# Kernel optimization log

Measured on AMD Instinct MI355X. Metric: run time of the kernel, lower is better.

Reference implementation:

```python
import jax, jax.numpy as jnp
import numpy as np

H, P, T = 256, 16, 4      # hidden_size, maxout_pool_size, max_dec_steps
B, M = 32, 600            # batch, document length

def _lstm_cell(x, h, c, W_ih, W_hh, b_ih, b_hh):
    g = x @ W_ih.T + b_ih + h @ W_hh.T + b_hh
    i, f, gg, o = jnp.split(g, 4, axis=1)  # torch gate order i,f,g,o
    c = jax.nn.sigmoid(f) * c + jax.nn.sigmoid(i) * jnp.tanh(gg)
    h = jax.nn.sigmoid(o) * jnp.tanh(c)
    return h, c

def _maxout(h, U, u_cat, mask_mult, W_lin, W1, b1, W2, b2, W12, b12):
    b, m, _ = U.shape
    r = jnp.tanh(jnp.concatenate([h, u_cat], axis=1) @ W_lin.T)                  # [b,H]
    m1_in = jnp.concatenate([U, jnp.broadcast_to(r[:, None, :], (b, m, H))], 2)  # [b,m,3H]
    m1 = (m1_in @ W1.T + b1).reshape(b, m, H, P).max(-1)                         # [b,m,H]
    m2 = (m1 @ W2.T + b2).reshape(b, m, H, P).max(-1)                            # [b,m,H]
    alpha = (jnp.concatenate([m1, m2], axis=2) @ W12.T + b12).max(-1)            # [b,m]
    return jax.nn.log_softmax(alpha + mask_mult, axis=1)

def _forward(U, d_mask, span, W_ih, W_hh, b_ih, b_hh,
             Ws_lin, Ws_m1, bs_m1, Ws_m2, bs_m2, Ws_m12, bs_m12,
             We_lin, We_m1, be_m1, We_m2, be_m2, We_m12, be_m12):
    b, m, _ = U.shape
    idxb = jnp.arange(b)
    mask_mult = (1.0 - d_mask.astype(U.dtype)) * -1e30
    s_i = jnp.zeros(b, jnp.int32)
    e_i = (jnp.sum(d_mask, 1) - 1).astype(jnp.int32)
    s_tgt, e_tgt = span[:, 0], span[:, 1]
    h = jnp.zeros((b, H), U.dtype)
    c = jnp.zeros((b, H), U.dtype)
    mask_s = mask_e = None
    res_s, res_e, res_ms, res_me, losses = [], [], [], [], []
    u_s = U[idxb, s_i]
    for t in range(T):
        u_e = U[idxb, e_i]
        u_cat = jnp.concatenate([u_s, u_e], axis=1)
        h, c = _lstm_cell(u_cat, h, c, W_ih, W_hh, b_ih, b_hh)
        # start pointer
        lsm = _maxout(h, U, u_cat, mask_mult, Ws_lin, Ws_m1, bs_m1, Ws_m2, bs_m2, Ws_m12, bs_m12)
        idx = jnp.argmax(lsm, axis=1).astype(jnp.int32)
        if t == 0:
            mask_s = jnp.ones(b, bool)
        else:
            idx = idx * mask_s.astype(jnp.int32)
            prev = s_i * mask_s.astype(jnp.int32)
            mask_s = idx != prev
        loss_s = jnp.mean(-jnp.take_along_axis(lsm, s_tgt[:, None], 1)[:, 0]) * mask_s.astype(U.dtype)
        s_i = idx
        u_s = U[idxb, s_i]
        # end pointer
        u_cat2 = jnp.concatenate([u_s, u_e], axis=1)
        lsm_e = _maxout(h, U, u_cat2, mask_mult, We_lin, We_m1, be_m1, We_m2, be_m2, We_m12, be_m12)
        idx_e = jnp.argmax(lsm_e, axis=1).astype(jnp.int32)
        if t == 0:
            mask_e = jnp.ones(b, bool)
        else:
            idx_e = idx_e * mask_e.astype(jnp.int32)
            prev_e = e_i * mask_e.astype(jnp.int32)
            mask_e = idx_e != prev_e
        loss_e = jnp.mean(-jnp.take_along_axis(lsm_e, e_tgt[:, None], 1)[:, 0]) * mask_e.astype(U.dtype)
        e_i = idx_e
        losses.append(loss_s + loss_e)
        res_s.append(s_i); res_ms.append(mask_s)
        res_e.append(e_i); res_me.append(mask_e)
    pos_s = jnp.sum(jnp.stack(res_ms, 1).astype(jnp.int32), 1) - 1
    p1 = jnp.take_along_axis(jnp.stack(res_s, 1), pos_s[:, None], 1)[:, 0]
    pos_e = jnp.sum(jnp.stack(res_me, 1).astype(jnp.int32), 1) - 1
    p2 = jnp.take_along_axis(jnp.stack(res_e, 1), pos_e[:, None], 1)[:, 0]
    loss = jnp.mean(jnp.sum(jnp.stack(losses, 1), 1) / T)
    return loss, p1, p2

def setup_inputs():
    key = jax.random.key(0)
    ks = jax.random.split(key, 16)
    U = jax.random.normal(ks[0], (B, M, 2 * H), jnp.float32)
    lengths = jax.random.randint(ks[1], (B,), M // 2, M + 1)
    d_mask = (jnp.arange(M)[None, :] < lengths[:, None]).astype(jnp.int32)
    span = jax.random.randint(ks[2], (B, 2), 0, M // 2).astype(jnp.int32)
    def w(k, shape, fan_in):
        return (jax.random.normal(k, shape, jnp.float32) / np.float32(np.sqrt(fan_in)))
    b_ih = jnp.zeros(4 * H, jnp.float32).at[H:2 * H].set(1.0)  # forget-gate bias init
    params = {
        'W_ih': w(ks[3], (4 * H, 4 * H), 4 * H), 'W_hh': w(ks[4], (4 * H, H), H),
        'b_ih': b_ih, 'b_hh': jnp.zeros(4 * H, jnp.float32),
        'Ws_lin': w(ks[5], (H, 5 * H), 5 * H),
        'Ws_m1': w(ks[6], (H * P, 3 * H), 3 * H), 'bs_m1': jnp.zeros(H * P, jnp.float32),
        'Ws_m2': w(ks[7], (H * P, H), H), 'bs_m2': jnp.zeros(H * P, jnp.float32),
        'Ws_m12': w(ks[8], (P, 2 * H), 2 * H), 'bs_m12': jnp.zeros(P, jnp.float32),
        'We_lin': w(ks[9], (H, 5 * H), 5 * H),
        'We_m1': w(ks[10], (H * P, 3 * H), 3 * H), 'be_m1': jnp.zeros(H * P, jnp.float32),
        'We_m2': w(ks[11], (H * P, H), H), 'be_m2': jnp.zeros(H * P, jnp.float32),
        'We_m12': w(ks[12], (P, 2 * H), 2 * H), 'be_m12': jnp.zeros(P, jnp.float32),
    }
    return {'U': U, 'd_mask': d_mask, 'span': span, **params}

def reference(U, d_mask, span, W_ih, W_hh, b_ih, b_hh,
              Ws_lin, Ws_m1, bs_m1, Ws_m2, bs_m2, Ws_m12, bs_m12,
              We_lin, We_m1, be_m1, We_m2, be_m2, We_m12, be_m12):
    return _forward(U, d_mask, span, W_ih, W_hh, b_ih, b_hh,
                    Ws_lin, Ws_m1, bs_m1, Ws_m2, bs_m2, Ws_m12, bs_m12,
                    We_lin, We_m1, be_m1, We_m2, be_m2, We_m12, be_m12)
```

## Files before the change

kernel.cpp:

```cpp
#include <hip/hip_runtime.h>
#include <math.h>

namespace {

typedef unsigned short u16;
typedef __attribute__((ext_vector_type(4))) float f32x4;
typedef __attribute__((ext_vector_type(8))) _Float16 f16x8;
typedef __attribute__((ext_vector_type(4))) _Float16 f16x4;

constexpr int B = 32;
constexpr int M = 600;
constexpr int H = 256;
constexpr int TSTEPS = 4;
constexpr int HP = 4096;
constexpr int BM = B * M;
constexpr int TWOH = 512;
constexpr int THREEH = 768;
constexpr int FOURH = 1024;
constexpr int FIVEH = 1280;
constexpr int NTILES = BM / 128;

__device__ __forceinline__ float sigf(float x) { return 1.0f / (1.0f + expf(-x)); }

__device__ __forceinline__ void gload16(const u16* g, u16* l) {
    __builtin_amdgcn_global_load_lds(
        (const __attribute__((address_space(1))) void*)g,
        (__attribute__((address_space(3))) void*)l, 16, 0, 0);
}

__global__ void k_init(const int* __restrict__ d_mask,
                       float* __restrict__ h, float* __restrict__ c,
                       float* __restrict__ loss_vec,
                       int* __restrict__ s_i, int* __restrict__ e_i,
                       int* __restrict__ p1r, int* __restrict__ p2r)
{
    int tid = threadIdx.x;
    for (int i = tid; i < B * H; i += 256) { h[i] = 0.f; c[i] = 0.f; }
    if (tid < B) {
        loss_vec[tid] = 0.f;
        s_i[tid] = 0;
        int s = 0;
        const int* row = d_mask + tid * M;
        for (int m = 0; m < M; ++m) s += row[m];
        e_i[tid] = s - 1;
        p1r[tid] = 0; p2r[tid] = 0;
    }
}

__global__ __launch_bounds__(128) void k_flags(const int* __restrict__ d_mask,
                                               int* __restrict__ flags)
{
    int bm = blockIdx.x * 128 + threadIdx.x;
    int cnt = __syncthreads_count(d_mask[bm]);
    if (threadIdx.x == 0) flags[blockIdx.x] = (cnt == 0) ? 1 : 0;
}

__global__ __launch_bounds__(256) void k_gather(
    const float* __restrict__ U, const int* __restrict__ s_i,
    const int* __restrict__ e_i, float* __restrict__ u_cat)
{
    int idx = blockIdx.x * 256 + threadIdx.x;
    int b = idx >> 9, k = idx & 511;
    u_cat[b * FOURH + k]       = U[((size_t)b * M + s_i[b]) * TWOH + k];
    u_cat[b * FOURH + 512 + k] = U[((size_t)b * M + e_i[b]) * TWOH + k];
}

__global__ __launch_bounds__(256) void k_lstm_gemm2(
    const float* __restrict__ U, const int* __restrict__ s_i,
    const int* __restrict__ e_i, const float* __restrict__ h,
    const float* __restrict__ W_ih, const float* __restrict__ W_hh,
    const float* __restrict__ b_ih, const float* __restrict__ b_hh,
    float* __restrict__ g)
{
    int idx = blockIdx.x * 256 + threadIdx.x;
    int b = idx >> 10, j = idx & 1023;
    const float* us = U + ((size_t)b * M + s_i[b]) * TWOH;
    const float* ue = U + ((size_t)b * M + e_i[b]) * TWOH;
    float acc = 0.f;
    const float4* x4 = (const float4*)us;
    const float4* wi4 = (const float4*)(W_ih + (size_t)j * FOURH);
    #pragma unroll 4
    for (int k = 0; k < TWOH / 4; ++k) {
        float4 a = x4[k], w = wi4[k];
        acc += a.x * w.x + a.y * w.y + a.z * w.z + a.w * w.w;
    }
    const float4* y4 = (const float4*)ue;
    const float4* wi4b = wi4 + TWOH / 4;
    #pragma unroll 4
    for (int k = 0; k < TWOH / 4; ++k) {
        float4 a = y4[k], w = wi4b[k];
        acc += a.x * w.x + a.y * w.y + a.z * w.z + a.w * w.w;
    }
    const float4* h4 = (const float4*)(h + b * H);
    const float4* wh4 = (const float4*)(W_hh + (size_t)j * H);
    #pragma unroll 4
    for (int k = 0; k < H / 4; ++k) {
        float4 a = h4[k], w = wh4[k];
        acc += a.x * w.x + a.y * w.y + a.z * w.z + a.w * w.w;
    }
    g[idx] = acc + b_ih[j] + b_hh[j];
}

__global__ __launch_bounds__(256) void k_lstm_gemm(
    const float* __restrict__ u_cat, const float* __restrict__ h,
    const float* __restrict__ W_ih, const float* __restrict__ W_hh,
    const float* __restrict__ b_ih, const float* __restrict__ b_hh,
    float* __restrict__ g)
{
    int idx = blockIdx.x * 256 + threadIdx.x;
    int b = idx >> 10, j = idx & 1023;
    float acc = 0.f;
    const float4* x4 = (const float4*)(u_cat + b * FOURH);
    const float4* wi4 = (const float4*)(W_ih + (size_t)j * FOURH);
    #pragma unroll 4
    for (int k = 0; k < FOURH / 4; ++k) {
        float4 a = x4[k], w = wi4[k];
        acc += a.x * w.x + a.y * w.y + a.z * w.z + a.w * w.w;
    }
    const float4* h4 = (const float4*)(h + b * H);
    const float4* wh4 = (const float4*)(W_hh + (size_t)j * H);
    #pragma unroll 4
    for (int k = 0; k < H / 4; ++k) {
        float4 a = h4[k], w = wh4[k];
        acc += a.x * w.x + a.y * w.y + a.z * w.z + a.w * w.w;
    }
    g[idx] = acc + b_ih[j] + b_hh[j];
}

__global__ __launch_bounds__(256) void k_lstm_gates(
    const float* __restrict__ g, float* __restrict__ h, float* __restrict__ c)
{
    int idx = blockIdx.x * 256 + threadIdx.x;
    int b = idx >> 8, i = idx & (H - 1);
    const float* gr = g + b * FOURH;
    float gi = gr[i], gf = gr[H + i], gg = gr[2 * H + i], go = gr[3 * H + i];
    float cn = sigf(gf) * c[idx] + sigf(gi) * tanhf(gg);
    c[idx] = cn;
    h[idx] = sigf(go) * tanhf(cn);
}

__global__ __launch_bounds__(256) void k_r2(
    const float* __restrict__ h, const float* __restrict__ U,
    const int* __restrict__ s_i, const int* __restrict__ e_i,
    const float* __restrict__ W_lin, float* __restrict__ r)
{
    int idx = blockIdx.x * 256 + threadIdx.x;
    int b = idx >> 8, i = idx & (H - 1);
    const float* w = W_lin + (size_t)i * FIVEH;
    float acc = 0.f;
    const float4* h4 = (const float4*)(h + b * H);
    const float4* w4 = (const float4*)w;
    #pragma unroll 4
    for (int k = 0; k < H / 4; ++k) {
        float4 a = h4[k], ww = w4[k];
        acc += a.x * ww.x + a.y * ww.y + a.z * ww.z + a.w * ww.w;
    }
    const float4* x4 = (const float4*)(U + ((size_t)b * M + s_i[b]) * TWOH);
    const float4* w4b = (const float4*)(w + H);
    #pragma unroll 4
    for (int k = 0; k < TWOH / 4; ++k) {
        float4 a = x4[k], ww = w4b[k];
        acc += a.x * ww.x + a.y * ww.y + a.z * ww.z + a.w * ww.w;
    }
    const float4* y4 = (const float4*)(U + ((size_t)b * M + e_i[b]) * TWOH);
    const float4* w4c = (const float4*)(w + H + TWOH);
    #pragma unroll 4
    for (int k = 0; k < TWOH / 4; ++k) {
        float4 a = y4[k], ww = w4c[k];
        acc += a.x * ww.x + a.y * ww.y + a.z * ww.z + a.w * ww.w;
    }
    r[idx] = tanhf(acc);
}

__global__ __launch_bounds__(256) void k_r(
    const float* __restrict__ h, const float* __restrict__ u_cat,
    const float* __restrict__ W_lin, float* __restrict__ r)
{
    int idx = blockIdx.x * 256 + threadIdx.x;
    int b = idx >> 8, i = idx & (H - 1);
    const float* w = W_lin + (size_t)i * FIVEH;
    float acc = 0.f;
    const float4* h4 = (const float4*)(h + b * H);
    const float4* w4 = (const float4*)w;
    #pragma unroll 4
    for (int k = 0; k < H / 4; ++k) {
        float4 a = h4[k], ww = w4[k];
        acc += a.x * ww.x + a.y * ww.y + a.z * ww.z + a.w * ww.w;
    }
    const float4* x4 = (const float4*)(u_cat + b * FOURH);
    const float4* w4b = (const float4*)(w + H);
    #pragma unroll 4
    for (int k = 0; k < FOURH / 4; ++k) {
        float4 a = x4[k], ww = w4b[k];
        acc += a.x * ww.x + a.y * ww.y + a.z * ww.z + a.w * ww.w;
    }
    r[idx] = tanhf(acc);
}

__global__ __launch_bounds__(256) void k_rW(
    const float* __restrict__ r, const float* __restrict__ W1,
    const float* __restrict__ b1, float* __restrict__ rW)
{
    int idx = blockIdx.x * 256 + threadIdx.x;
    int b = idx >> 12, j = idx & (HP - 1);
    const float4* r4 = (const float4*)(r + b * H);
    const float4* w4 = (const float4*)(W1 + (size_t)j * THREEH + TWOH);
    float acc = 0.f;
    #pragma unroll 4
    for (int k = 0; k < H / 4; ++k) {
        float4 a = r4[k], w = w4[k];
        acc += a.x * w.x + a.y * w.y + a.z * w.z + a.w * w.w;
    }
    rW[idx] = acc + b1[j];
}

__global__ __launch_bounds__(256) void k_rW2(
    const float* __restrict__ r, const float* __restrict__ Wt,
    const float* __restrict__ b1, float* __restrict__ rW)
{
    const int b = blockIdx.y;
    const int j = blockIdx.x * 256 + threadIdx.x;
    __shared__ float sr[256];
    sr[threadIdx.x] = r[b * H + threadIdx.x];
    __syncthreads();
    float acc = b1[j];
    #pragma unroll 4
    for (int k = 0; k < H; ++k) acc += sr[k] * Wt[(size_t)k * HP + j];
    rW[(size_t)b * HP + j] = acc;
}

__global__ __launch_bounds__(256) void k_transp(
    const float* __restrict__ W, float* __restrict__ Wt)
{
    int idx = blockIdx.x * 256 + threadIdx.x;
    int k = idx >> 12, j = idx & (HP - 1);
    Wt[idx] = W[(size_t)j * THREEH + TWOH + k];
}

__global__ __launch_bounds__(256) void k_cvtH(
    const float* __restrict__ src, int ld, int Kc, _Float16* __restrict__ dst)
{
    int i4 = blockIdx.x * 256 + threadIdx.x;
    int perrow = Kc >> 2;
    int row = i4 / perrow;
    int kc = (i4 - row * perrow) << 2;
    float4 v = *(const float4*)(src + (size_t)row * ld + kc);
    f16x4 o;
    o[0] = (_Float16)v.x; o[1] = (_Float16)v.y; o[2] = (_Float16)v.z; o[3] = (_Float16)v.w;
    *(f16x4*)(dst + (size_t)row * Kc + kc) = o;
}

template <int EPI>
__global__ __launch_bounds__(256, 4) void gemmJ(
    const _Float16* __restrict__ A, const _Float16* __restrict__ Bw,
    int K, const float* __restrict__ extra, const int* __restrict__ skip,
    float* __restrict__ Cf, _Float16* __restrict__ Ch)
{
    if (skip[blockIdx.y]) return;
    __shared__ __align__(16) u16 sA[2][128 * 32];
    __shared__ __align__(16) u16 sB[2][128 * 32];
    const int tid = threadIdx.x;
    const int w = tid >> 6, lane = tid & 63;
    const int row0 = blockIdx.y * 128, col0 = blockIdx.x * 128;
    const int wm = w & 1, wn = w >> 1;

    const int r1g = tid >> 2,        k1 = (tid & 3) ^ ((r1g >> 1) & 3);
    const int r2g = (tid + 256) >> 2, k2 = ((tid + 256) & 3) ^ ((r2g >> 1) & 3);
    const size_t gA1 = (size_t)(row0 + r1g) * K + k1 * 8;
    const size_t gA2 = (size_t)(row0 + r2g) * K + k2 * 8;
    const size_t gB1 = (size_t)(col0 + r1g) * K + k1 * 8;
    const size_t gB2 = (size_t)(col0 + r2g) * K + k2 * 8;

    f32x4 acc[4][4] = {};

    gload16((const u16*)(A  + gA1), &sA[0][tid * 8]);
    gload16((const u16*)(A  + gA2), &sA[0][(tid + 256) * 8]);
    gload16((const u16*)(Bw + gB1), &sB[0][tid * 8]);
    gload16((const u16*)(Bw + gB2), &sB[0][(tid + 256) * 8]);

    const int iters = K >> 5;
    const int mrow = lane & 15;
    const int kg = lane >> 4;
    const int slot = kg ^ ((mrow >> 1) & 3);
    const int eoff = slot << 3;

    for (int it = 0; it < iters; ++it) {
        const int cur = it & 1;
        __syncthreads();
        if (it + 1 < iters) {
            const int k0n = (it + 1) << 5;
            gload16((const u16*)(A  + gA1 + k0n), &sA[1 - cur][tid * 8]);
            gload16((const u16*)(A  + gA2 + k0n), &sA[1 - cur][(tid + 256) * 8]);
            gload16((const u16*)(Bw + gB1 + k0n), &sB[1 - cur][tid * 8]);
            gload16((const u16*)(Bw + gB2 + k0n), &sB[1 - cur][(tid + 256) * 8]);
        }
        const u16* pa = &sA[cur][(wm * 64 + mrow) * 32 + eoff];
        const u16* pb = &sB[cur][(wn * 64 + mrow) * 32 + eoff];
        f16x8 fa[4], fb[4];
        #pragma unroll
        for (int f = 0; f < 4; ++f) {
            fa[f] = *(const f16x8*)(pa + f * 16 * 32);
            fb[f] = *(const f16x8*)(pb + f * 16 * 32);
        }
        #pragma unroll
        for (int i = 0; i < 4; ++i) {
            #pragma unroll
            for (int j = 0; j < 4; ++j) {
                acc[i][j] = __builtin_amdgcn_mfma_f32_16x16x32_f16(fa[i], fb[j], acc[i][j], 0, 0, 0);
            }
        }
    }

    const int cq = lane & 15, rq = lane >> 4;
    if (EPI == 4) {
        #pragma unroll
        for (int i = 0; i < 4; ++i) {
            #pragma unroll
            for (int j = 0; j < 4; ++j) {
                int col = col0 + wn * 64 + j * 16 + cq;
                #pragma unroll
                for (int rr = 0; rr < 4; ++rr) {
                    int row = row0 + wm * 64 + i * 16 + rq * 4 + rr;
                    Ch[(size_t)row * HP + col] = (_Float16)acc[i][j][rr];
                }
            }
        }
    } else if (EPI == 1) {
        #pragma unroll
        for (int j = 0; j < 4; ++j) {
            int col = col0 + wn * 64 + j * 16 + cq;
            int gcol = (col0 >> 4) + wn * 4 + j;
            float bv = extra[col];
            #pragma unroll
            for (int i = 0; i < 4; ++i) {
                #pragma unroll
                for (int rr = 0; rr < 4; ++rr) {
                    float v = acc[i][j][rr] + bv;
                    v = fmaxf(v, __shfl_xor(v, 1));
                    v = fmaxf(v, __shfl_xor(v, 2));
                    v = fmaxf(v, __shfl_xor(v, 4));
                    v = fmaxf(v, __shfl_xor(v, 8));
                    if (cq == 0) {
                        int row = row0 + wm * 64 + i * 16 + rq * 4 + rr;
                        Cf[(size_t)row * H + gcol] = v;
                    }
                }
            }
        }
    } else {
        #pragma unroll
        for (int j = 0; j < 4; ++j) {
            int col = col0 + wn * 64 + j * 16 + cq;
            int gcol = (col0 >> 4) + wn * 4 + j;
            #pragma unroll
            for (int i = 0; i < 4; ++i) {
                #pragma unroll
                for (int rr = 0; rr < 4; ++rr) {
                    int row = row0 + wm * 64 + i * 16 + rq * 4 + rr;
                    int b = row / M;
                    float v = acc[i][j][rr] + extra[(size_t)b * HP + col];
                    v = fmaxf(v, __shfl_xor(v, 1));
                    v = fmaxf(v, __shfl_xor(v, 2));
                    v = fmaxf(v, __shfl_xor(v, 4));
                    v = fmaxf(v, __shfl_xor(v, 8));
                    if (cq == 0)
                        Ch[(size_t)row * H + gcol] = (_Float16)v;
                }
            }
        }
    }
}

__global__ __launch_bounds__(256) void k_m1A16(
    const _Float16* __restrict__ A, const float* __restrict__ rW,
    _Float16* __restrict__ m1)
{
    int idx = blockIdx.x * 256 + threadIdx.x;
    int bm = idx >> 8;
    int h = idx & (H - 1);
    int b = bm / M;
    const f16x8* a8 = (const f16x8*)(A + (size_t)bm * HP + (h << 4));
    const float4* r4 = (const float4*)(rW + (size_t)b * HP + (h << 4));
    f16x8 a0 = a8[0], a1 = a8[1];
    float4 ra = r4[0], rb = r4[1], rc = r4[2], rd = r4[3];
    float mx;
    mx = fmaxf(fmaxf(fmaxf((float)a0[0] + ra.x, (float)a0[1] + ra.y),
                     fmaxf((float)a0[2] + ra.z, (float)a0[3] + ra.w)),
         fmaxf(fmaxf((float)a0[4] + rb.x, (float)a0[5] + rb.y),
               fmaxf((float)a0[6] + rb.z, (float)a0[7] + rb.w)));
    mx = fmaxf(mx,
         fmaxf(fmaxf(fmaxf((float)a1[0] + rc.x, (float)a1[1] + rc.y),
                     fmaxf((float)a1[2] + rc.z, (float)a1[3] + rc.w)),
               fmaxf(fmaxf((float)a1[4] + rd.x, (float)a1[5] + rd.y),
                     fmaxf((float)a1[6] + rd.z, (float)a1[7] + rd.w))));
    m1[idx] = (_Float16)mx;
}

template <int EPI>
__global__ __launch_bounds__(256) void gemm64(
    const float* __restrict__ Ag, int lda,
    const float* __restrict__ Bg, int ldb,
    const float* __restrict__ extra,
    float* __restrict__ C, int K, int ldc)
{
    __shared__ float As[16][68];
    __shared__ float Bs[16][68];
    const int tid = threadIdx.x;
    const int tx = tid & 15;
    const int ty = tid >> 4;
    const int row0 = blockIdx.y * 64;
    const int col0 = blockIdx.x * 64;
    const int lr = tid >> 2;
    const int lk = (tid & 3) << 2;
    const float* Aload = Ag + (size_t)(row0 + lr) * lda + lk;
    const float* Bload = Bg + (size_t)(col0 + lr) * ldb + lk;
    float acc[4][4] = {};
    for (int k0 = 0; k0 < K; k0 += 16) {
        float4 av = *(const float4*)(Aload + k0);
        float4 bv = *(const float4*)(Bload + k0);
        __syncthreads();
        As[lk + 0][lr] = av.x; As[lk + 1][lr] = av.y; As[lk + 2][lr] = av.z; As[lk + 3][lr] = av.w;
        Bs[lk + 0][lr] = bv.x; Bs[lk + 1][lr] = bv.y; Bs[lk + 2][lr] = bv.z; Bs[lk + 3][lr] = bv.w;
        __syncthreads();
        #pragma unroll
        for (int k = 0; k < 16; ++k) {
            float4 a4 = *(const float4*)(&As[k][ty << 2]);
            float4 b4 = *(const float4*)(&Bs[k][tx << 2]);
            acc[0][0] += a4.x * b4.x; acc[0][1] += a4.x * b4.y; acc[0][2] += a4.x * b4.z; acc[0][3] += a4.x * b4.w;
            acc[1][0] += a4.y * b4.x; acc[1][1] += a4.y * b4.y; acc[1][2] += a4.y * b4.z; acc[1][3] += a4.y * b4.w;
            acc[2][0] += a4.z * b4.x; acc[2][1] += a4.z * b4.y; acc[2][2] += a4.z * b4.z; acc[2][3] += a4.z * b4.w;
            acc[3][0] += a4.w * b4.x; acc[3][1] += a4.w * b4.y; acc[3][2] += a4.w * b4.z; acc[3][3] += a4.w * b4.w;
        }
    }
    if (EPI == 1) {
        const int cb = col0 + (tx << 2);
        float b0 = extra[cb], b1v = extra[cb + 1], b2v = extra[cb + 2], b3v = extra[cb + 3];
        #pragma unroll
        for (int i = 0; i < 4; ++i) {
            float mth = fmaxf(fmaxf(acc[i][0] + b0, acc[i][1] + b1v),
                              fmaxf(acc[i][2] + b2v, acc[i][3] + b3v));
            float r1 = fmaxf(mth, __shfl_xor(mth, 1));
            float r2 = fmaxf(r1, __shfl_xor(r1, 2));
            if ((tx & 3) == 0)
                C[(size_t)(row0 + (ty << 2) + i) * ldc + (col0 >> 4) + (tx >> 2)] = r2;
        }
    } else if (EPI == 2) {
        const int cb = col0 + (tx << 2);
        #pragma unroll
        for (int i = 0; i < 4; ++i) {
            int row = row0 + (ty << 2) + i;
            int b = row / M;
            const float* rw = extra + (size_t)b * HP + cb;
            float mth = fmaxf(fmaxf(acc[i][0] + rw[0], acc[i][1] + rw[1]),
                              fmaxf(acc[i][2] + rw[2], acc[i][3] + rw[3]));
            float r1 = fmaxf(mth, __shfl_xor(mth, 1));
            float r2 = fmaxf(r1, __shfl_xor(r1, 2));
            if ((tx & 3) == 0)
                C[(size_t)row * ldc + (col0 >> 4) + (tx >> 2)] = r2;
        }
    }
}

__global__ __launch_bounds__(256) void k_alpha(
    const float* __restrict__ m1, const float* __restrict__ m2,
    const float* __restrict__ W12, const float* __restrict__ b12,
    const int* __restrict__ d_mask, float* __restrict__ alpha)
{
    __shared__ float Ws[16 * 512];
    const int tid = threadIdx.x;
    for (int i = tid; i < 16 * 512; i += 256) Ws[i] = W12[i];
    __syncthreads();
    const int wave = tid >> 6, lane = tid & 63;
    const int bm = blockIdx.x * 4 + wave;
    const float* r1 = m1 + (size_t)bm * H;
    const float* r2 = m2 + (size_t)bm * H;
    float acc[16] = {};
    #pragma unroll
    for (int q = 0; q < 4; ++q) {
        int k = lane + (q << 6);
        float x = r1[k];
        #pragma unroll
        for (int p = 0; p < 16; ++p) acc[p] += x * Ws[p * 512 + k];
    }
    #pragma unroll
    for (int q = 0; q < 4; ++q) {
        int k = lane + (q << 6);
        float x = r2[k];
        #pragma unroll
        for (int p = 0; p < 16; ++p) acc[p] += x * Ws[p * 512 + 256 + k];
    }
    #pragma unroll
    for (int p = 0; p < 16; ++p) {
        float v = acc[p];
        v += __shfl_xor(v, 1);  v += __shfl_xor(v, 2);  v += __shfl_xor(v, 4);
        v += __shfl_xor(v, 8);  v += __shfl_xor(v, 16); v += __shfl_xor(v, 32);
        acc[p] = v;
    }
    if (lane == 0) {
        float mx = -INFINITY;
        #pragma unroll
        for (int p = 0; p < 16; ++p) mx = fmaxf(mx, acc[p] + b12[p]);
        alpha[bm] = d_mask[bm] ? mx : -1e30f;
    }
}

__global__ __launch_bounds__(256) void k_alpha2(
    const _Float16* __restrict__ m1, const float* __restrict__ m2,
    const float* __restrict__ W12, const float* __restrict__ b12,
    const int* __restrict__ d_mask, float* __restrict__ alpha)
{
    __shared__ float Ws[16 * 512];
    const int tid = threadIdx.x;
    for (int i = tid; i < 16 * 512; i += 256) Ws[i] = W12[i];
    __syncthreads();
    const int wave = tid >> 6, lane = tid & 63;
    const int bm0 = blockIdx.x * 16 + wave * 4;
    for (int rr = 0; rr < 4; ++rr) {
        const int bm = bm0 + rr;
        if (!d_mask[bm]) {
            if (lane == 0) alpha[bm] = -1e30f;
            continue;
        }
        const _Float16* r1 = m1 + (size_t)bm * H;
        const float* r2 = m2 + (size_t)bm * H;
        float acc[16] = {};
        #pragma unroll
        for (int q = 0; q < 4; ++q) {
            int k = lane + (q << 6);
            float x = (float)r1[k];
            #pragma unroll
            for (int p = 0; p < 16; ++p) acc[p] += x * Ws[p * 512 + k];
        }
        #pragma unroll
        for (int q = 0; q < 4; ++q) {
            int k = lane + (q << 6);
            float x = r2[k];
            #pragma unroll
            for (int p = 0; p < 16; ++p) acc[p] += x * Ws[p * 512 + 256 + k];
        }
        #pragma unroll
        for (int p = 0; p < 16; ++p) {
            float v = acc[p];
            v += __shfl_xor(v, 1);  v += __shfl_xor(v, 2);  v += __shfl_xor(v, 4);
            v += __shfl_xor(v, 8);  v += __shfl_xor(v, 16); v += __shfl_xor(v, 32);
            acc[p] = v;
        }
        if (lane == 0) {
            float mx = -INFINITY;
            #pragma unroll
            for (int p = 0; p < 16; ++p) mx = fmaxf(mx, acc[p] + b12[p]);
            alpha[bm] = mx;
        }
    }
}

__global__ __launch_bounds__(1024) void k_smu(
    const float* __restrict__ alpha, const int* __restrict__ span, int phase,
    int* __restrict__ pos, int* __restrict__ mask,
    int* __restrict__ prun, float* __restrict__ loss_vec, int t)
{
    __shared__ float s_loss[B];
    __shared__ int s_idx[B];
    const int wave = threadIdx.x >> 6, lane = threadIdx.x & 63;
    for (int b = wave; b < B; b += 16) {
        const float* row = alpha + b * M;
        float best = -INFINITY; int bidx = 0;
        for (int m = lane; m < M; m += 64) {
            float v = row[m];
            if (v > best) { best = v; bidx = m; }
        }
        #pragma unroll
        for (int off = 1; off < 64; off <<= 1) {
            float v2 = __shfl_xor(best, off);
            int i2 = __shfl_xor(bidx, off);
            if (v2 > best || (v2 == best && i2 < bidx)) { best = v2; bidx = i2; }
        }
        float ps = 0.f;
        for (int m = lane; m < M; m += 64) ps += expf(row[m] - best);
        #pragma unroll
        for (int off = 32; off > 0; off >>= 1) ps += __shfl_xor(ps, off);
        if (lane == 0) {
            float lse = best + logf(ps);
            int tgt = span[b * 2 + phase];
            s_loss[b] = -(row[tgt] - lse);
            s_idx[b] = bidx;
        }
    }
    __syncthreads();
    if (wave == 0) {
        int b = lane;
        int active = (b < B) ? 1 : 0;
        int ni = 0, nm = 0;
        if (active) {
            int id = s_idx[b];
            if (t == 0) { nm = 1; ni = id; }
            else {
                int om = mask[b];
                ni = id * om;
                int prev = pos[b] * om;
                nm = (ni != prev) ? 1 : 0;
            }
        }
        float v = active ? s_loss[b] : 0.f;
        #pragma unroll
        for (int off = 32; off > 0; off >>= 1) v += __shfl_xor(v, off);
        float S = v * (1.0f / (float)B);
        if (active) {
            pos[b] = ni;
            mask[b] = nm;
            if (nm) { prun[b] = ni; loss_vec[b] += S; }
        }
    }
}

__global__ __launch_bounds__(256) void k_softmax(
    const float* __restrict__ alpha, const int* __restrict__ span, int phase,
    float* __restrict__ loss_term, int* __restrict__ idx_out)
{
    __shared__ float sv[256];
    __shared__ int si[256];
    const int b = blockIdx.x, tid = threadIdx.x;
    const float* row = alpha + b * M;
    float best = -INFINITY; int bidx = 0;
    for (int m = tid; m < M; m += 256) {
        float v = row[m];
        if (v > best) { best = v; bidx = m; }
    }
    sv[tid] = best; si[tid] = bidx;
    __syncthreads();
    for (int s = 128; s > 0; s >>= 1) {
        if (tid < s) {
            float v2 = sv[tid + s]; int i2 = si[tid + s];
            if (v2 > sv[tid] || (v2 == sv[tid] && i2 < si[tid])) { sv[tid] = v2; si[tid] = i2; }
        }
        __syncthreads();
    }
    float bmax = sv[0]; int amax = si[0];
    __syncthreads();
    float ps = 0.f;
    for (int m = tid; m < M; m += 256) ps += expf(row[m] - bmax);
    sv[tid] = ps;
    __syncthreads();
    for (int s = 128; s > 0; s >>= 1) {
        if (tid < s) sv[tid] += sv[tid + s];
        __syncthreads();
    }
    if (tid == 0) {
        float lse = bmax + logf(sv[0]);
        int tgt = span[b * 2 + phase];
        loss_term[b] = -(row[tgt] - lse);
        idx_out[b] = amax;
    }
}

__global__ void k_update(const int* __restrict__ idx_in, const float* __restrict__ loss_term,
                         int* __restrict__ pos, int* __restrict__ mask,
                         int* __restrict__ prun, float* __restrict__ loss_vec, int t)
{
    int b = threadIdx.x;
    int active = (b < B) ? 1 : 0;
    int ni = 0, nm = 0;
    if (active) {
        int id = idx_in[b];
        if (t == 0) { nm = 1; ni = id; }
        else {
            int om = mask[b];
            ni = id * om;
            int prev = pos[b] * om;
            nm = (ni != prev) ? 1 : 0;
        }
    }
    float v = active ? loss_term[b] : 0.f;
    #pragma unroll
    for (int off = 32; off > 0; off >>= 1) v += __shfl_xor(v, off);
    float S = v * (1.0f / (float)B);
    if (active) {
        pos[b] = ni;
        mask[b] = nm;
        if (nm) { prun[b] = ni; loss_vec[b] += S; }
    }
}

__global__ void k_finalize(const float* __restrict__ loss_vec, const int* __restrict__ p1r,
                           const int* __restrict__ p2r, float* __restrict__ out)
{
    int b = threadIdx.x;
    float v = (b < B) ? loss_vec[b] : 0.f;
    #pragma unroll
    for (int off = 32; off > 0; off >>= 1) v += __shfl_xor(v, off);
    if (b == 0) out[0] = v / (float)(B * TSTEPS);
    if (b < B) {
        out[1 + b] = (float)p1r[b];
        out[1 + B + b] = (float)p2r[b];
    }
}

}

extern "C" void kernel_launch(void* const* d_in, const int* in_sizes, int n_in,
                              void* d_out, int out_size, void* d_ws, size_t ws_size,
                              hipStream_t stream)
{
    const float* U      = (const float*)d_in[0];
    const int*   d_mask = (const int*)d_in[1];
    const int*   span   = (const int*)d_in[2];
    const float* W_ih   = (const float*)d_in[3];
    const float* W_hh   = (const float*)d_in[4];
    const float* b_ih   = (const float*)d_in[5];
    const float* b_hh   = (const float*)d_in[6];
    const float* Ws_lin = (const float*)d_in[7];
    const float* Ws_m1  = (const float*)d_in[8];
    const float* bs_m1  = (const float*)d_in[9];
    const float* Ws_m2  = (const float*)d_in[10];
    const float* bs_m2  = (const float*)d_in[11];
    const float* Ws_m12 = (const float*)d_in[12];
    const float* bs_m12 = (const float*)d_in[13];
    const float* We_lin = (const float*)d_in[14];
    const float* We_m1  = (const float*)d_in[15];
    const float* be_m1  = (const float*)d_in[16];
    const float* We_m2  = (const float*)d_in[17];
    const float* be_m2  = (const float*)d_in[18];
    const float* We_m12 = (const float*)d_in[19];
    const float* be_m12 = (const float*)d_in[20];

    float* ws = (float*)d_ws;
    size_t o = 0;
    float* m2b   = ws + o; o += (size_t)BM * H;
    float* alphab= ws + o; o += BM;
    float* u_cat = ws + o; o += B * FOURH;
    float* gbuf  = ws + o; o += B * FOURH;
    float* hbuf  = ws + o; o += B * H;
    float* cbuf  = ws + o; o += B * H;
    float* rbuf  = ws + o; o += B * H;
    float* rWb   = ws + o; o += B * HP;
    float* loss_term = ws + o; o += B;
    float* loss_vec  = ws + o; o += B;
    int* ib = (int*)(ws + o); o += 8 * B + 160;
    int* idxb   = ib + 0 * B;
    int* s_i    = ib + 1 * B;
    int* e_i    = ib + 2 * B;
    int* mask_s = ib + 3 * B;
    int* mask_e = ib + 4 * B;
    int* p1r    = ib + 5 * B;
    int* p2r    = ib + 6 * B;
    int* flags  = ib + 8 * B;
    size_t o_common = (o + 3) & ~(size_t)3;

    float* m1b = ws + o_common;

    size_t p = o_common;
    float* Wt_s = ws + p; p += (size_t)H * HP;
    float* Wt_e = ws + p; p += (size_t)H * HP;
    _Float16* hs = (_Float16*)(ws + p);
    size_t q = 0;
    _Float16* Uh  = hs + q; q += (size_t)BM * TWOH;
    _Float16* W1s = hs + q; q += (size_t)HP * TWOH;
    _Float16* W1e = hs + q; q += (size_t)HP * TWOH;
    _Float16* W2s = hs + q; q += (size_t)HP * H;
    _Float16* W2e = hs + q; q += (size_t)HP * H;
    _Float16* m1b16 = hs + q; q += (size_t)BM * H;
    q = (q + 7) & ~(size_t)7;
    const size_t need2 = p * sizeof(float) + q * sizeof(_Float16);
    _Float16* A_s16 = hs + q;
    _Float16* A_e16 = A_s16 + (size_t)BM * HP;
    const size_t need15s = need2 + (size_t)BM * HP * sizeof(_Float16);
    const size_t need16  = need15s + (size_t)BM * HP * sizeof(_Float16);

    const int tier = (ws_size >= need16) ? 16
                   : (ws_size >= need15s) ? 15
                   : (ws_size >= need2) ? 2 : 3;

    k_init<<<1, 256, 0, stream>>>(d_mask, hbuf, cbuf, loss_vec, s_i, e_i, p1r, p2r);

    if (tier != 3) {
        k_flags<<<NTILES, 128, 0, stream>>>(d_mask, flags);
        k_cvtH<<<BM * TWOH / 4 / 256, 256, 0, stream>>>(U, TWOH, TWOH, Uh);
        k_cvtH<<<HP * TWOH / 4 / 256, 256, 0, stream>>>(Ws_m1, THREEH, TWOH, W1s);
        k_cvtH<<<HP * TWOH / 4 / 256, 256, 0, stream>>>(We_m1, THREEH, TWOH, W1e);
        k_cvtH<<<HP * H / 4 / 256, 256, 0, stream>>>(Ws_m2, H, H, W2s);
        k_cvtH<<<HP * H / 4 / 256, 256, 0, stream>>>(We_m2, H, H, W2e);
        k_transp<<<HP * H / 256, 256, 0, stream>>>(Ws_m1, Wt_s);
        k_transp<<<HP * H / 256, 256, 0, stream>>>(We_m1, Wt_e);

        dim3 gJ(HP / 128, NTILES);
        if (tier >= 15) {
            gemmJ<4><<<gJ, 256, 0, stream>>>(Uh, W1s, TWOH, nullptr, flags, nullptr, A_s16);
        }
        if (tier == 16) {
            gemmJ<4><<<gJ, 256, 0, stream>>>(Uh, W1e, TWOH, nullptr, flags, nullptr, A_e16);
        }

        for (int t = 0; t < TSTEPS; ++t) {
            k_lstm_gemm2<<<128, 256, 0, stream>>>(U, s_i, e_i, hbuf, W_ih, W_hh, b_ih, b_hh, gbuf);
            k_lstm_gates<<<32, 256, 0, stream>>>(gbuf, hbuf, cbuf);

            k_r2<<<32, 256, 0, stream>>>(hbuf, U, s_i, e_i, Ws_lin, rbuf);
            k_rW2<<<dim3(HP / 256, B), 256, 0, stream>>>(rbuf, Wt_s, bs_m1, rWb);
            if (tier >= 15)
                k_m1A16<<<BM * H / 256, 256, 0, stream>>>(A_s16, rWb, m1b16);
            else
                gemmJ<3><<<gJ, 256, 0, stream>>>(Uh, W1s, TWOH, rWb, flags, nullptr, m1b16);
            gemmJ<1><<<gJ, 256, 0, stream>>>(m1b16, W2s, H, bs_m2, flags, m2b, nullptr);
            k_alpha2<<<BM / 16, 256, 0, stream>>>(m1b16, m2b, Ws_m12, bs_m12, d_mask, alphab);
            k_smu<<<1, 1024, 0, stream>>>(alphab, span, 0, s_i, mask_s, p1r, loss_vec, t);

            k_r2<<<32, 256, 0, stream>>>(hbuf, U, s_i, e_i, We_lin, rbuf);
            k_rW2<<<dim3(HP / 256, B), 256, 0, stream>>>(rbuf, Wt_e, be_m1, rWb);
            if (tier == 16)
                k_m1A16<<<BM * H / 256, 256, 0, stream>>>(A_e16, rWb, m1b16);
            else
                gemmJ<3><<<gJ, 256, 0, stream>>>(Uh, W1e, TWOH, rWb, flags, nullptr, m1b16);
            gemmJ<1><<<gJ, 256, 0, stream>>>(m1b16, W2e, H, be_m2, flags, m2b, nullptr);
            k_alpha2<<<BM / 16, 256, 0, stream>>>(m1b16, m2b, We_m12, be_m12, d_mask, alphab);
            k_smu<<<1, 1024, 0, stream>>>(alphab, span, 1, e_i, mask_e, p2r, loss_vec, t);
        }
    } else {
        dim3 gemm_grid(HP / 64, BM / 64);
        for (int t = 0; t < TSTEPS; ++t) {
            k_gather<<<64, 256, 0, stream>>>(U, s_i, e_i, u_cat);
            k_lstm_gemm<<<128, 256, 0, stream>>>(u_cat, hbuf, W_ih, W_hh, b_ih, b_hh, gbuf);
            k_lstm_gates<<<32, 256, 0, stream>>>(gbuf, hbuf, cbuf);

            k_r<<<32, 256, 0, stream>>>(hbuf, u_cat, Ws_lin, rbuf);
            k_rW<<<512, 256, 0, stream>>>(rbuf, Ws_m1, bs_m1, rWb);
            gemm64<2><<<gemm_grid, 256, 0, stream>>>(U, TWOH, Ws_m1, THREEH, rWb, m1b, TWOH, H);
            gemm64<1><<<gemm_grid, 256, 0, stream>>>(m1b, H, Ws_m2, H, bs_m2, m2b, H, H);
            k_alpha<<<BM / 4, 256, 0, stream>>>(m1b, m2b, Ws_m12, bs_m12, d_mask, alphab);
            k_softmax<<<B, 256, 0, stream>>>(alphab, span, 0, loss_term, idxb);
            k_update<<<1, 64, 0, stream>>>(idxb, loss_term, s_i, mask_s, p1r, loss_vec, t);

            k_gather<<<64, 256, 0, stream>>>(U, s_i, e_i, u_cat);

            k_r<<<32, 256, 0, stream>>>(hbuf, u_cat, We_lin, rbuf);
            k_rW<<<512, 256, 0, stream>>>(rbuf, We_m1, be_m1, rWb);
            gemm64<2><<<gemm_grid, 256, 0, stream>>>(U, TWOH, We_m1, THREEH, rWb, m1b, TWOH, H);
            gemm64<1><<<gemm_grid, 256, 0, stream>>>(m1b, H, We_m2, H, be_m2, m2b, H, H);
            k_alpha<<<BM / 4, 256, 0, stream>>>(m1b, m2b, We_m12, be_m12, d_mask, alphab);
            k_softmax<<<B, 256, 0, stream>>>(alphab, span, 1, loss_term, idxb);
            k_update<<<1, 64, 0, stream>>>(idxb, loss_term, e_i, mask_e, p2r, loss_vec, t);
        }
    }

    k_finalize<<<1, 64, 0, stream>>>(loss_vec, p1r, p2r, (float*)d_out);
}
```

Baseline: 2.878 ms.

## Split r projection across lanes, tile weight transpose, store m2 as fp16

Splits the r-projection dot product four ways per output with shuffle reduction and launches four times more blocks, so the small kernel gets more parallelism. Replaces the strided weight transpose with a shared-memory tiled transpose for coalesced reads and writes. Stores the m2 maxout result as fp16 instead of fp32, which halves its write and read traffic in the alpha kernel at some cost in precision. Also hoists the per-row batch bias lookup in the gemm epilogue into two preloaded values selected by a row boundary.

Result: faster. 2.511 ms (-12.8%).

```diff
diff --git a/kernel.cpp b/kernel.cpp
--- a/kernel.cpp
+++ b/kernel.cpp
@@ -144,6 +144,34 @@
     const int* __restrict__ s_i, const int* __restrict__ e_i,
     const float* __restrict__ W_lin, float* __restrict__ r)
 {
+    int gid = blockIdx.x * 256 + threadIdx.x;
+    int out = gid >> 2;
+    int part = gid & 3;
+    int b = out >> 8, i = out & (H - 1);
+    const float4* w4 = (const float4*)(W_lin + (size_t)i * FIVEH);
+    const float4* h4 = (const float4*)(h + b * H);
+    const float4* us4 = (const float4*)(U + ((size_t)b * M + s_i[b]) * TWOH);
+    const float4* ue4 = (const float4*)(U + ((size_t)b * M + e_i[b]) * TWOH);
+    float acc = 0.f;
+    int k0 = part * 80;
+    #pragma unroll 4
+    for (int kk = k0; kk < k0 + 80; ++kk) {
+        float4 a;
+        if (kk < 64) a = h4[kk];
+        else if (kk < 192) a = us4[kk - 64];
+        else a = ue4[kk - 192];
+        float4 ww = w4[kk];
+        acc += a.x * ww.x + a.y * ww.y + a.z * ww.z + a.w * ww.w;
+    }
+    acc += __shfl_xor(acc, 1);
+    acc += __shfl_xor(acc, 2);
+    if (part == 0) r[out] = tanhf(acc);
+}
+
+__global__ __launch_bounds__(256) void k_r(
+    const float* __restrict__ h, const float* __restrict__ u_cat,
+    const float* __restrict__ W_lin, float* __restrict__ r)
+{
     int idx = blockIdx.x * 256 + threadIdx.x;
     int b = idx >> 8, i = idx & (H - 1);
     const float* w = W_lin + (size_t)i * FIVEH;
@@ -155,38 +183,6 @@
         float4 a = h4[k], ww = w4[k];
         acc += a.x * ww.x + a.y * ww.y + a.z * ww.z + a.w * ww.w;
     }
-    const float4* x4 = (const float4*)(U + ((size_t)b * M + s_i[b]) * TWOH);
-    const float4* w4b = (const float4*)(w + H);
-    #pragma unroll 4
-    for (int k = 0; k < TWOH / 4; ++k) {
-        float4 a = x4[k], ww = w4b[k];
-        acc += a.x * ww.x + a.y * ww.y + a.z * ww.z + a.w * ww.w;
-    }
-    const float4* y4 = (const float4*)(U + ((size_t)b * M + e_i[b]) * TWOH);
-    const float4* w4c = (const float4*)(w + H + TWOH);
-    #pragma unroll 4
-    for (int k = 0; k < TWOH / 4; ++k) {
-        float4 a = y4[k], ww = w4c[k];
-        acc += a.x * ww.x + a.y * ww.y + a.z * ww.z + a.w * ww.w;
-    }
-    r[idx] = tanhf(acc);
-}
-
-__global__ __launch_bounds__(256) void k_r(
-    const float* __restrict__ h, const float* __restrict__ u_cat,
-    const float* __restrict__ W_lin, float* __restrict__ r)
-{
-    int idx = blockIdx.x * 256 + threadIdx.x;
-    int b = idx >> 8, i = idx & (H - 1);
-    const float* w = W_lin + (size_t)i * FIVEH;
-    float acc = 0.f;
-    const float4* h4 = (const float4*)(h + b * H);
-    const float4* w4 = (const float4*)w;
-    #pragma unroll 4
-    for (int k = 0; k < H / 4; ++k) {
-        float4 a = h4[k], ww = w4[k];
-        acc += a.x * ww.x + a.y * ww.y + a.z * ww.z + a.w * ww.w;
-    }
     const float4* x4 = (const float4*)(u_cat + b * FOURH);
     const float4* w4b = (const float4*)(w + H);
     #pragma unroll 4
@@ -229,12 +225,24 @@
     rW[(size_t)b * HP + j] = acc;
 }
 
-__global__ __launch_bounds__(256) void k_transp(
+__global__ __launch_bounds__(256) void k_transp2(
     const float* __restrict__ W, float* __restrict__ Wt)
 {
-    int idx = blockIdx.x * 256 + threadIdx.x;
-    int k = idx >> 12, j = idx & (HP - 1);
-    Wt[idx] = W[(size_t)j * THREEH + TWOH + k];
+    __shared__ float s[32][33];
+    int j0 = (blockIdx.x & 127) << 5;
+    int k0 = (blockIdx.x >> 7) << 5;
+    int tx = threadIdx.x & 31, ty = threadIdx.x >> 5;
+    #pragma unroll
+    for (int kk = 0; kk < 4; ++kk) {
+        int jl = ty + kk * 8;
+        s[jl][tx] = W[(size_t)(j0 + jl) * THREEH + TWOH + k0 + tx];
+    }
+    __syncthreads();
+    #pragma unroll
+    for (int kk = 0; kk < 4; ++kk) {
+        int kl = ty + kk * 8;
+        Wt[(size_t)(k0 + kl) * HP + j0 + tx] = s[tx][kl];
+    }
 }
 
 __global__ __launch_bounds__(256) void k_cvtH(
@@ -342,23 +350,27 @@
                     v = fmaxf(v, __shfl_xor(v, 8));
                     if (cq == 0) {
                         int row = row0 + wm * 64 + i * 16 + rq * 4 + rr;
-                        Cf[(size_t)row * H + gcol] = v;
+                        Ch[(size_t)row * H + gcol] = (_Float16)v;
                     }
                 }
             }
         }
     } else {
+        const int rbase = row0 + wm * 64;
+        const int b0 = rbase / M;
+        const int bnd = (b0 + 1) * M;
         #pragma unroll
         for (int j = 0; j < 4; ++j) {
             int col = col0 + wn * 64 + j * 16 + cq;
             int gcol = (col0 >> 4) + wn * 4 + j;
+            float e0 = extra[(size_t)b0 * HP + col];
+            float e1 = extra[(size_t)(b0 + 1) * HP + col];
             #pragma unroll
             for (int i = 0; i < 4; ++i) {
                 #pragma unroll
                 for (int rr = 0; rr < 4; ++rr) {
-                    int row = row0 + wm * 64 + i * 16 + rq * 4 + rr;
-                    int b = row / M;
-                    float v = acc[i][j][rr] + extra[(size_t)b * HP + col];
+                    int row = rbase + i * 16 + rq * 4 + rr;
+                    float v = acc[i][j][rr] + ((row >= bnd) ? e1 : e0);
                     v = fmaxf(v, __shfl_xor(v, 1));
                     v = fmaxf(v, __shfl_xor(v, 2));
                     v = fmaxf(v, __shfl_xor(v, 4));
@@ -505,7 +517,7 @@
 }
 
 __global__ __launch_bounds__(256) void k_alpha2(
-    const _Float16* __restrict__ m1, const float* __restrict__ m2,
+    const _Float16* __restrict__ m1, const _Float16* __restrict__ m2,
     const float* __restrict__ W12, const float* __restrict__ b12,
     const int* __restrict__ d_mask, float* __restrict__ alpha)
 {
@@ -522,7 +534,7 @@
             continue;
         }
         const _Float16* r1 = m1 + (size_t)bm * H;
-        const float* r2 = m2 + (size_t)bm * H;
+        const _Float16* r2 = m2 + (size_t)bm * H;
         float acc[16] = {};
         #pragma unroll
         for (int q = 0; q < 4; ++q) {
@@ -534,7 +546,7 @@
         #pragma unroll
         for (int q = 0; q < 4; ++q) {
             int k = lane + (q << 6);
-            float x = r2[k];
+            float x = (float)r2[k];
             #pragma unroll
             for (int p = 0; p < 16; ++p) acc[p] += x * Ws[p * 512 + 256 + k];
         }
@@ -766,6 +778,8 @@
     const size_t need15s = need2 + (size_t)BM * HP * sizeof(_Float16);
     const size_t need16  = need15s + (size_t)BM * HP * sizeof(_Float16);
 
+    _Float16* m2h = (_Float16*)m2b;
+
     const int tier = (ws_size >= need16) ? 16
                    : (ws_size >= need15s) ? 15
                    : (ws_size >= need2) ? 2 : 3;
@@ -779,8 +793,8 @@
         k_cvtH<<<HP * TWOH / 4 / 256, 256, 0, stream>>>(We_m1, THREEH, TWOH, W1e);
         k_cvtH<<<HP * H / 4 / 256, 256, 0, stream>>>(Ws_m2, H, H, W2s);
         k_cvtH<<<HP * H / 4 / 256, 256, 0, stream>>>(We_m2, H, H, W2e);
-        k_transp<<<HP * H / 256, 256, 0, stream>>>(Ws_m1, Wt_s);
-        k_transp<<<HP * H / 256, 256, 0, stream>>>(We_m1, Wt_e);
+        k_transp2<<<1024, 256, 0, stream>>>(Ws_m1, Wt_s);
+        k_transp2<<<1024, 256, 0, stream>>>(We_m1, Wt_e);
 
         dim3 gJ(HP / 128, NTILES);
         if (tier >= 15) {
@@ -794,24 +808,24 @@
             k_lstm_gemm2<<<128, 256, 0, stream>>>(U, s_i, e_i, hbuf, W_ih, W_hh, b_ih, b_hh, gbuf);
             k_lstm_gates<<<32, 256, 0, stream>>>(gbuf, hbuf, cbuf);
 
-            k_r2<<<32, 256, 0, stream>>>(hbuf, U, s_i, e_i, Ws_lin, rbuf);
+            k_r2<<<128, 256, 0, stream>>>(hbuf, U, s_i, e_i, Ws_lin, rbuf);
             k_rW2<<<dim3(HP / 256, B), 256, 0, stream>>>(rbuf, Wt_s, bs_m1, rWb);
             if (tier >= 15)
                 k_m1A16<<<BM * H / 256, 256, 0, stream>>>(A_s16, rWb, m1b16);
             else
                 gemmJ<3><<<gJ, 256, 0, stream>>>(Uh, W1s, TWOH, rWb, flags, nullptr, m1b16);
-            gemmJ<1><<<gJ, 256, 0, stream>>>(m1b16, W2s, H, bs_m2, flags, m2b, nullptr);
-            k_alpha2<<<BM / 16, 256, 0, stream>>>(m1b16, m2b, Ws_m12, bs_m12, d_mask, alphab);
+            gemmJ<1><<<gJ, 256, 0, stream>>>(m1b16, W2s, H, bs_m2, flags, nullptr, m2h);
+            k_alpha2<<<BM / 16, 256, 0, stream>>>(m1b16, m2h, Ws_m12, bs_m12, d_mask, alphab);
             k_smu<<<1, 1024, 0, stream>>>(alphab, span, 0, s_i, mask_s, p1r, loss_vec, t);
 
-            k_r2<<<32, 256, 0, stream>>>(hbuf, U, s_i, e_i, We_lin, rbuf);
+            k_r2<<<128, 256, 0, stream>>>(hbuf, U, s_i, e_i, We_lin, rbuf);
             k_rW2<<<dim3(HP / 256, B), 256, 0, stream>>>(rbuf, Wt_e, be_m1, rWb);
             if (tier == 16)
                 k_m1A16<<<BM * H / 256, 256, 0, stream>>>(A_e16, rWb, m1b16);
             else
                 gemmJ<3><<<gJ, 256, 0, stream>>>(Uh, W1e, TWOH, rWb, flags, nullptr, m1b16);
-            gemmJ<1><<<gJ, 256, 0, stream>>>(m1b16, W2e, H, be_m2, flags, m2b, nullptr);
-            k_alpha2<<<BM / 16, 256, 0, stream>>>(m1b16, m2b, We_m12, be_m12, d_mask, alphab);
+            gemmJ<1><<<gJ, 256, 0, stream>>>(m1b16, W2e, H, be_m2, flags, nullptr, m2h);
+            k_alpha2<<<BM / 16, 256, 0, stream>>>(m1b16, m2h, We_m12, be_m12, d_mask, alphab);
             k_smu<<<1, 1024, 0, stream>>>(alphab, span, 1, e_i, mask_e, p2r, loss_vec, t);
         }
     } else {
```
